# Kernel optimization log

Measured on AMD Instinct MI355X. Metric: run time of the kernel, lower is better.

## Reference

```python
import jax, jax.numpy as jnp
import numpy as np

TOP_K = 2

def setup_inputs() -> dict:
    key = jax.random.key(0)
    k1, k2, k3, k4, k5 = jax.random.split(key, 5)
    B, S, D, E, H = 1, 2048, 2048, 8, 5632
    scale = 0.02
    return {
        "x": jax.random.normal(k1, (B, S, D), dtype=jnp.float32),
        "gate_w": jax.random.normal(k2, (E, D), dtype=jnp.float32) * scale,
        "w1": jax.random.normal(k3, (E, H, D), dtype=jnp.float32) * scale,
        "w2": jax.random.normal(k4, (E, D, H), dtype=jnp.float32) * scale,
        "w3": jax.random.normal(k5, (E, H, D), dtype=jnp.float32) * scale,
    }


def reference(x, gate_w, w1, w2, w3):
    # x: [B, S, D]; gate_w: [E, D]; w1/w3: [E, H, D]; w2: [E, D, H]
    B, S, D = x.shape
    E = gate_w.shape[0]
    xf = x.reshape(-1, D)                      # [T, D]
    T = xf.shape[0]

    # Gate (gate_softmax=False): topk on raw scores, softmax over the top-k
    scores = xf @ gate_w.T                     # [T, E]
    expert_weights, expert_indices = jax.lax.top_k(scores, TOP_K)
    expert_weights = jax.nn.softmax(expert_weights, axis=-1)  # [T, K]

    # Scatter top-k weights to a dense [T, E] combine matrix (zeros elsewhere)
    combine = jnp.zeros((T, E), dtype=xf.dtype).at[
        jnp.arange(T)[:, None], expert_indices
    ].add(expert_weights)

    # SwiGLU FFN per expert, batched over the (small, fixed) expert axis.
    # Math identical to masked dispatch since combine is zero off the top-k.
    h = jax.nn.silu(jnp.einsum("td,ehd->eth", xf, w1)) \
        * jnp.einsum("td,ehd->eth", xf, w3)    # [E, T, H]
    ye = jnp.einsum("eth,edh->etd", h, w2)     # [E, T, D]

    # Weighted combine of top-k expert outputs per token
    y = jnp.einsum("etd,te->td", ye, combine)  # [T, D]
    return y.reshape(B, S, D)
```

## Files before the change

kernel.cpp:

```cpp
#include <hip/hip_runtime.h>
#include <hip/hip_bf16.h>

#define T_TOK 2048
#define DIM   2048
#define NE    8
#define NH    5632

typedef __attribute__((ext_vector_type(4))) float f32x4;
typedef __attribute__((ext_vector_type(8))) short short8;
typedef __attribute__((ext_vector_type(4))) unsigned int u32x4;
typedef __attribute__((ext_vector_type(4))) float float4v;

__device__ inline unsigned short f2bf(float f) {
    unsigned u = __builtin_bit_cast(unsigned, f);
    u += 0x7fffu + ((u >> 16) & 1u);
    return (unsigned short)(u >> 16);
}

__device__ __forceinline__ void glds16(const void* g, void* l) {
    __builtin_amdgcn_global_load_lds((const __attribute__((address_space(1))) void*)g,
                                     (__attribute__((address_space(3))) void*)l, 16, 0, 0);
}

__global__ void k_cvt(const float* __restrict__ src, unsigned short* __restrict__ dst, int n8) {
    int i = blockIdx.x * blockDim.x + threadIdx.x;
    if (i >= n8) return;
    const float4v* xv = (const float4v*)src;
    float4v a = xv[2 * i], b = xv[2 * i + 1];
    short8 o;
    o[0] = (short)f2bf(a[0]); o[1] = (short)f2bf(a[1]);
    o[2] = (short)f2bf(a[2]); o[3] = (short)f2bf(a[3]);
    o[4] = (short)f2bf(b[0]); o[5] = (short)f2bf(b[1]);
    o[6] = (short)f2bf(b[2]); o[7] = (short)f2bf(b[3]);
    ((short8*)dst)[i] = o;
}

__global__ void k_gate(const float* __restrict__ x, const float* __restrict__ gw,
                       int* __restrict__ rt_e, float* __restrict__ rt_w, int* __restrict__ cnt) {
    int wid = threadIdx.x >> 6, lane = threadIdx.x & 63;
    int t = blockIdx.x * 4 + wid;
    if (t >= T_TOK) return;
    float acc[NE];
#pragma unroll
    for (int e = 0; e < NE; e++) acc[e] = 0.f;
    const float* xr = x + (size_t)t * DIM;
    for (int d = lane; d < DIM; d += 64) {
        float xv = xr[d];
#pragma unroll
        for (int e = 0; e < NE; e++) acc[e] += xv * gw[e * DIM + d];
    }
#pragma unroll
    for (int e = 0; e < NE; e++) {
        float v = acc[e];
#pragma unroll
        for (int off = 32; off; off >>= 1) v += __shfl_xor(v, off);
        acc[e] = v;
    }
    if (lane == 0) {
        int i0 = 0; float s0 = acc[0];
#pragma unroll
        for (int e = 1; e < NE; e++) if (acc[e] > s0) { s0 = acc[e]; i0 = e; }
        int i1 = -1; float s1 = -1e30f;
#pragma unroll
        for (int e = 0; e < NE; e++) if (e != i0 && acc[e] > s1) { s1 = acc[e]; i1 = e; }
        float w0 = 1.f / (1.f + expf(s1 - s0));
        rt_e[2 * t] = i0; rt_e[2 * t + 1] = i1;
        rt_w[2 * t] = w0; rt_w[2 * t + 1] = 1.f - w0;
        atomicAdd(&cnt[i0], 1);
        atomicAdd(&cnt[i1], 1);
    }
}

__global__ void k_base(const int* __restrict__ cnt, int* __restrict__ base, int* __restrict__ pb) {
    if (threadIdx.x == 0) {
        int s = 0, p = 0;
        for (int e = 0; e < NE; e++) {
            base[e] = s; pb[e] = p;
            s += cnt[e];
            p += ((cnt[e] + 127) >> 7) << 7;
        }
    }
}

__global__ void k_assign(const int* __restrict__ rt_e, const float* __restrict__ rt_w,
                         const int* __restrict__ base, int* __restrict__ run,
                         int* __restrict__ tok, float* __restrict__ tw) {
    int t = blockIdx.x * blockDim.x + threadIdx.x;
    if (t >= T_TOK) return;
#pragma unroll
    for (int k = 0; k < 2; k++) {
        int e = rt_e[2 * t + k];
        int p = atomicAdd(&run[e], 1);
        int g = base[e] + p;
        tok[g] = t;
        tw[g] = rt_w[2 * t + k];
    }
}

__global__ void k_packw13(const float* __restrict__ w1, const float* __restrict__ w3,
                          unsigned short* __restrict__ w1p, unsigned short* __restrict__ w3p) {
    int z = blockIdx.z;
    const float* src = (z < 8) ? w1 : w3;
    unsigned short* dst = (z < 8) ? w1p : w3p;
    int e = z & 7, nt = blockIdx.y, kt = blockIdx.x;
    int lane = threadIdx.x & 63, w = threadIdx.x >> 6;
    int kc = lane & 7;
    const float* sb = src + (size_t)e * NH * DIM;
    unsigned short* db = dst + ((size_t)(e * 88 + nt) * 32 + kt) * 4096;
#pragma unroll
    for (int it = 0; it < 2; ++it) {
        int rloc = it * 32 + w * 8 + (lane >> 3);
        const float* s = sb + (size_t)(nt * 64 + rloc) * DIM + kt * 64 + kc * 8;
        float4v a = *(const float4v*)s, b = *(const float4v*)(s + 4);
        short8 o;
        o[0]=(short)f2bf(a[0]); o[1]=(short)f2bf(a[1]); o[2]=(short)f2bf(a[2]); o[3]=(short)f2bf(a[3]);
        o[4]=(short)f2bf(b[0]); o[5]=(short)f2bf(b[1]); o[6]=(short)f2bf(b[2]); o[7]=(short)f2bf(b[3]);
        *(short8*)(db + kc * 512 + rloc * 8) = o;
    }
}

__global__ void k_packw2(const float* __restrict__ w2, unsigned short* __restrict__ w2p) {
    int e = blockIdx.z, nt = blockIdx.y, kt = blockIdx.x;
    int lane = threadIdx.x & 63, w = threadIdx.x >> 6;
    int kc = lane & 7;
    const float* sb = w2 + (size_t)e * DIM * NH;
    unsigned short* db = w2p + ((size_t)(e * 16 + nt) * 88 + kt) * 8192;
#pragma unroll
    for (int it = 0; it < 4; ++it) {
        int rloc = it * 32 + w * 8 + (lane >> 3);
        const float* s = sb + (size_t)(nt * 128 + rloc) * NH + kt * 64 + kc * 8;
        float4v a = *(const float4v*)s, b = *(const float4v*)(s + 4);
        short8 o;
        o[0]=(short)f2bf(a[0]); o[1]=(short)f2bf(a[1]); o[2]=(short)f2bf(a[2]); o[3]=(short)f2bf(a[3]);
        o[4]=(short)f2bf(b[0]); o[5]=(short)f2bf(b[1]); o[6]=(short)f2bf(b[2]); o[7]=(short)f2bf(b[3]);
        *(short8*)(db + kc * 1024 + rloc * 8) = o;
    }
}

__global__ void k_xpack(const float* __restrict__ x,
                        const int* __restrict__ cnt, const int* __restrict__ base,
                        const int* __restrict__ pb, const int* __restrict__ tok,
                        unsigned short* __restrict__ xp) {
    int e = blockIdx.z, mt = blockIdx.y, kt = blockIdx.x;
    int c = cnt[e], m0 = mt * 128;
    if (m0 >= c) return;
    int gb = base[e];
    int ptile = (pb[e] >> 7) + mt;
    int lane = threadIdx.x & 63, w = threadIdx.x >> 6;
    int kc = lane & 7;
    unsigned short* db = xp + (size_t)ptile * 262144 + (size_t)kt * 8192;
#pragma unroll
    for (int it = 0; it < 4; ++it) {
        int rloc = it * 32 + w * 8 + (lane >> 3);
        int slot = m0 + rloc;
        int t = tok[gb + (slot < c ? slot : 0)];
        const float* s = x + (size_t)t * DIM + kt * 64 + kc * 8;
        float4v a = *(const float4v*)s, b = *(const float4v*)(s + 4);
        short8 o;
        o[0]=(short)f2bf(a[0]); o[1]=(short)f2bf(a[1]); o[2]=(short)f2bf(a[2]); o[3]=(short)f2bf(a[3]);
        o[4]=(short)f2bf(b[0]); o[5]=(short)f2bf(b[1]); o[6]=(short)f2bf(b[2]); o[7]=(short)f2bf(b[3]);
        *(short8*)(db + kc * 1024 + rloc * 8) = o;
    }
}

__launch_bounds__(256, 4)
__global__ void k_ffn1(const unsigned short* __restrict__ xp,
                       const unsigned short* __restrict__ w1p, const unsigned short* __restrict__ w3p,
                       const int* __restrict__ cnt, const int* __restrict__ pb,
                       unsigned short* __restrict__ hb, int nwg) {
    int bid = blockIdx.x;
    int swz = (bid & 7) * (nwg >> 3) + (bid >> 3);
    int mt = swz & 15;
    int r2 = swz >> 4;
    int nt = r2 % 88;
    int e  = r2 / 88;
    int c  = cnt[e];
    int m0 = mt * 128;
    if (m0 >= c) return;
    int ptile = (pb[e] >> 7) + mt;

    __shared__ unsigned short As[8192];
    __shared__ unsigned short B1[4096];
    __shared__ unsigned short B3[4096];

    int tid = threadIdx.x;
    int lane = tid & 63, w = tid >> 6;
    int wm = w >> 1, wn = w & 1;
    int half = w & 1, wh = w >> 1;

    const unsigned short* aB  = xp  + (size_t)ptile * 262144 + half * 512 + lane * 8;
    const unsigned short* b1B = w1p + (size_t)(e * 88 + nt) * 131072 + lane * 8;
    const unsigned short* b3B = w3p + (size_t)(e * 88 + nt) * 131072 + lane * 8;

    f32x4 acc1[4][2], acc3[4][2];
#pragma unroll
    for (int i = 0; i < 4; i++)
#pragma unroll
        for (int j = 0; j < 2; j++) { acc1[i][j] = (f32x4)0.f; acc3[i][j] = (f32x4)0.f; }

    for (int kt = 0; kt < 32; ++kt) {
        __syncthreads();
#pragma unroll
        for (int i = 0; i < 4; i++) {
            int kc = i * 2 + wh;
            glds16(aB + kt * 8192 + kc * 1024, (char*)As + kc * 2048 + half * 1024);
        }
#pragma unroll
        for (int i = 0; i < 2; i++) {
            int kc = i * 4 + w;
            glds16(b1B + kt * 4096 + kc * 512, (char*)B1 + kc * 1024);
            glds16(b3B + kt * 4096 + kc * 512, (char*)B3 + kc * 1024);
        }
        asm volatile("s_waitcnt vmcnt(0)" ::: "memory");
        __syncthreads();
#pragma unroll
        for (int kh = 0; kh < 2; kh++) {
            int kc = kh * 4 + (lane >> 4);
            short8 a[4], b1[2], b3[2];
#pragma unroll
            for (int mf = 0; mf < 4; mf++) {
                int r = wm * 64 + mf * 16 + (lane & 15);
                a[mf] = *(const short8*)(As + kc * 1024 + r * 8);
            }
#pragma unroll
            for (int nf = 0; nf < 2; nf++) {
                int rb = wn * 32 + nf * 16 + (lane & 15);
                b1[nf] = *(const short8*)(B1 + kc * 512 + rb * 8);
                b3[nf] = *(const short8*)(B3 + kc * 512 + rb * 8);
            }
#pragma unroll
            for (int mf = 0; mf < 4; mf++)
#pragma unroll
                for (int nf = 0; nf < 2; nf++) {
                    acc1[mf][nf] = __builtin_amdgcn_mfma_f32_16x16x32_bf16(a[mf], b1[nf], acc1[mf][nf], 0, 0, 0);
                    acc3[mf][nf] = __builtin_amdgcn_mfma_f32_16x16x32_bf16(a[mf], b3[nf], acc3[mf][nf], 0, 0, 0);
                }
        }
    }

    unsigned short* hT = hb + ((size_t)ptile * 88 + nt) * 8192;
#pragma unroll
    for (int mf = 0; mf < 4; mf++)
#pragma unroll
        for (int nf = 0; nf < 2; nf++)
#pragma unroll
            for (int r = 0; r < 4; r++) {
                int row = wm * 64 + mf * 16 + ((lane >> 4) << 2) + r;
                int col = wn * 32 + nf * 16 + (lane & 15);
                if (m0 + row < c) {
                    float a = acc1[mf][nf][r];
                    float g = a / (1.f + expf(-a));
                    float v = g * acc3[mf][nf][r];
                    hT[(col >> 3) * 1024 + row * 8 + (col & 7)] = f2bf(v);
                }
            }
}

__launch_bounds__(256, 4)
__global__ void k_ffn2(const unsigned short* __restrict__ hb,
                       const unsigned short* __restrict__ w2p,
                       const int* __restrict__ cnt, const int* __restrict__ base,
                       const int* __restrict__ pb,
                       const int* __restrict__ tok, const float* __restrict__ tw,
                       float* __restrict__ y, int nwg) {
    int bid = blockIdx.x;
    int swz = (bid & 7) * (nwg >> 3) + (bid >> 3);
    int mt = swz & 15;
    int r2 = swz >> 4;
    int nt = r2 & 15;
    int e  = r2 >> 4;
    int c  = cnt[e];
    int m0 = mt * 128;
    if (m0 >= c) return;
    int gb = base[e];
    int ptile = (pb[e] >> 7) + mt;
    int n0 = nt * 128;

    __shared__ unsigned short As[8192];
    __shared__ unsigned short Bs[8192];
    __shared__ int   toks[128];
    __shared__ float gws[128];

    int tid = threadIdx.x;
    if (tid < 128) {
        int s = m0 + tid;
        toks[tid] = (s < c) ? tok[gb + s] : 0;
        gws[tid]  = (s < c) ? tw[gb + s] : 0.f;
    }

    int lane = tid & 63, w = tid >> 6;
    int wm = w >> 1, wn = w & 1;
    int half = w & 1, wh = w >> 1;

    const unsigned short* aB = hb  + (size_t)ptile * 720896 + half * 512 + lane * 8;
    const unsigned short* bB = w2p + (size_t)(e * 16 + nt) * 720896 + half * 512 + lane * 8;

    f32x4 acc[4][4];
#pragma unroll
    for (int i = 0; i < 4; i++)
#pragma unroll
        for (int j = 0; j < 4; j++) acc[i][j] = (f32x4)0.f;

    for (int kt = 0; kt < 88; ++kt) {
        __syncthreads();
#pragma unroll
        for (int i = 0; i < 4; i++) {
            int kc = i * 2 + wh;
            glds16(aB + kt * 8192 + kc * 1024, (char*)As + kc * 2048 + half * 1024);
            glds16(bB + kt * 8192 + kc * 1024, (char*)Bs + kc * 2048 + half * 1024);
        }
        asm volatile("s_waitcnt vmcnt(0)" ::: "memory");
        __syncthreads();
#pragma unroll
        for (int kh = 0; kh < 2; kh++) {
            int kc = kh * 4 + (lane >> 4);
            short8 a[4], b[4];
#pragma unroll
            for (int mf = 0; mf < 4; mf++) {
                int r = wm * 64 + mf * 16 + (lane & 15);
                a[mf] = *(const short8*)(As + kc * 1024 + r * 8);
            }
#pragma unroll
            for (int nf = 0; nf < 4; nf++) {
                int rb = wn * 64 + nf * 16 + (lane & 15);
                b[nf] = *(const short8*)(Bs + kc * 1024 + rb * 8);
            }
#pragma unroll
            for (int mf = 0; mf < 4; mf++)
#pragma unroll
                for (int nf = 0; nf < 4; nf++)
                    acc[mf][nf] = __builtin_amdgcn_mfma_f32_16x16x32_bf16(a[mf], b[nf], acc[mf][nf], 0, 0, 0);
        }
    }

#pragma unroll
    for (int mf = 0; mf < 4; mf++)
#pragma unroll
        for (int nf = 0; nf < 4; nf++)
#pragma unroll
            for (int r = 0; r < 4; r++) {
                int row = wm * 64 + mf * 16 + ((lane >> 4) << 2) + r;
                int col = wn * 64 + nf * 16 + (lane & 15);
                if (m0 + row < c) {
                    float v = gws[row] * acc[mf][nf][r];
                    atomicAdd(&y[(size_t)toks[row] * DIM + n0 + col], v);
                }
            }
}

__launch_bounds__(256)
__global__ void k_ffn1_fb(const unsigned short* __restrict__ xb,
                          const float* __restrict__ w1, const float* __restrict__ w3,
                          const int* __restrict__ cnt, const int* __restrict__ base,
                          const int* __restrict__ tok, unsigned short* __restrict__ hbuf) {
    int e  = blockIdx.x >> 4;
    int mt = blockIdx.x & 15;
    int c  = cnt[e];
    int m0 = mt * 128;
    if (m0 >= c) return;
    int gb = base[e];
    int n0 = blockIdx.y * 64;

    __shared__ unsigned short As[128 * 64];
    __shared__ unsigned short B1s[64 * 64];
    __shared__ unsigned short B3s[64 * 64];
    __shared__ int toks[128];

    int tid = threadIdx.x;
    if (tid < 128) {
        int s = m0 + tid;
        toks[tid] = (s < c) ? tok[gb + s] : tok[gb];
    }
    int lane = tid & 63, wid = tid >> 6;
    int wm = wid >> 1, wn = wid & 1;

    f32x4 acc1[4][2], acc3[4][2];
#pragma unroll
    for (int i = 0; i < 4; i++)
#pragma unroll
        for (int j = 0; j < 2; j++) { acc1[i][j] = (f32x4)0.f; acc3[i][j] = (f32x4)0.f; }

    const float* W1 = w1 + (size_t)e * NH * DIM + (size_t)n0 * DIM;
    const float* W3 = w3 + (size_t)e * NH * DIM + (size_t)n0 * DIM;

    for (int kt = 0; kt < DIM / 64; ++kt) {
        int k0 = kt * 64;
        __syncthreads();
#pragma unroll
        for (int i = 0; i < 4; i++) {
            int f = i * 256 + tid;
            int row = f >> 3, ch = f & 7;
            u32x4 v = *(const u32x4*)(xb + (size_t)toks[row] * DIM + k0 + ch * 8);
            *(u32x4*)(As + row * 64 + ((ch ^ (row & 7)) << 3)) = v;
        }
#pragma unroll
        for (int i = 0; i < 2; i++) {
            int f = i * 256 + tid;
            int row = f >> 3, ch = f & 7;
            {
                const float* src = W1 + (size_t)row * DIM + k0 + ch * 8;
                float4v a = *(const float4v*)src, b = *(const float4v*)(src + 4);
                short8 o;
                o[0]=(short)f2bf(a[0]); o[1]=(short)f2bf(a[1]); o[2]=(short)f2bf(a[2]); o[3]=(short)f2bf(a[3]);
                o[4]=(short)f2bf(b[0]); o[5]=(short)f2bf(b[1]); o[6]=(short)f2bf(b[2]); o[7]=(short)f2bf(b[3]);
                *(short8*)(B1s + row * 64 + ((ch ^ (row & 7)) << 3)) = o;
            }
            {
                const float* src = W3 + (size_t)row * DIM + k0 + ch * 8;
                float4v a = *(const float4v*)src, b = *(const float4v*)(src + 4);
                short8 o;
                o[0]=(short)f2bf(a[0]); o[1]=(short)f2bf(a[1]); o[2]=(short)f2bf(a[2]); o[3]=(short)f2bf(a[3]);
                o[4]=(short)f2bf(b[0]); o[5]=(short)f2bf(b[1]); o[6]=(short)f2bf(b[2]); o[7]=(short)f2bf(b[3]);
                *(short8*)(B3s + row * 64 + ((ch ^ (row & 7)) << 3)) = o;
            }
        }
        __syncthreads();
#pragma unroll
        for (int kk = 0; kk < 2; kk++) {
            int kch = kk * 4 + (lane >> 4);
            short8 af[4], b1f[2], b3f[2];
#pragma unroll
            for (int mf = 0; mf < 4; mf++) {
                int r = wm * 64 + mf * 16 + (lane & 15);
                af[mf] = *(const short8*)(As + r * 64 + ((kch ^ (r & 7)) << 3));
            }
#pragma unroll
            for (int nf = 0; nf < 2; nf++) {
                int r = wn * 32 + nf * 16 + (lane & 15);
                b1f[nf] = *(const short8*)(B1s + r * 64 + ((kch ^ (r & 7)) << 3));
                b3f[nf] = *(const short8*)(B3s + r * 64 + ((kch ^ (r & 7)) << 3));
            }
#pragma unroll
            for (int mf = 0; mf < 4; mf++)
#pragma unroll
                for (int nf = 0; nf < 2; nf++) {
                    acc1[mf][nf] = __builtin_amdgcn_mfma_f32_16x16x32_bf16(af[mf], b1f[nf], acc1[mf][nf], 0, 0, 0);
                    acc3[mf][nf] = __builtin_amdgcn_mfma_f32_16x16x32_bf16(af[mf], b3f[nf], acc3[mf][nf], 0, 0, 0);
                }
        }
    }
#pragma unroll
    for (int mf = 0; mf < 4; mf++)
#pragma unroll
        for (int nf = 0; nf < 2; nf++)
#pragma unroll
            for (int r = 0; r < 4; r++) {
                int row = wm * 64 + mf * 16 + ((lane >> 4) << 2) + r;
                int col = wn * 32 + nf * 16 + (lane & 15);
                if (m0 + row < c) {
                    float a = acc1[mf][nf][r];
                    float g = a / (1.f + expf(-a));
                    float v = g * acc3[mf][nf][r];
                    hbuf[(size_t)(gb + m0 + row) * NH + n0 + col] = f2bf(v);
                }
            }
}

__launch_bounds__(256)
__global__ void k_ffn2_fb(const unsigned short* __restrict__ hbuf,
                          const float* __restrict__ w2,
                          const int* __restrict__ cnt, const int* __restrict__ base,
                          const int* __restrict__ tok, const float* __restrict__ tw,
                          float* __restrict__ y) {
    int e  = blockIdx.x >> 4;
    int mt = blockIdx.x & 15;
    int c  = cnt[e];
    int m0 = mt * 128;
    if (m0 >= c) return;
    int gb = base[e];
    int n0 = blockIdx.y * 128;

    __shared__ unsigned short As[128 * 64];
    __shared__ unsigned short Bs[128 * 64];
    __shared__ int   toks[128];
    __shared__ float gws[128];

    int tid = threadIdx.x;
    if (tid < 128) {
        int s = m0 + tid;
        toks[tid] = (s < c) ? tok[gb + s] : 0;
        gws[tid]  = (s < c) ? tw[gb + s] : 0.f;
    }
    int lane = tid & 63, wid = tid >> 6;
    int wm = wid >> 1, wn = wid & 1;

    f32x4 acc[4][4];
#pragma unroll
    for (int i = 0; i < 4; i++)
#pragma unroll
        for (int j = 0; j < 4; j++) acc[i][j] = (f32x4)0.f;

    const float* W2 = w2 + (size_t)e * DIM * NH + (size_t)n0 * NH;

    for (int kt = 0; kt < NH / 64; ++kt) {
        int k0 = kt * 64;
        __syncthreads();
#pragma unroll
        for (int i = 0; i < 4; i++) {
            int f = i * 256 + tid;
            int row = f >> 3, ch = f & 7;
            int rr = m0 + row; rr = (rr < c) ? rr : (c - 1);
            u32x4 v = *(const u32x4*)(hbuf + (size_t)(gb + rr) * NH + k0 + ch * 8);
            *(u32x4*)(As + row * 64 + ((ch ^ (row & 7)) << 3)) = v;
        }
#pragma unroll
        for (int i = 0; i < 4; i++) {
            int f = i * 256 + tid;
            int row = f >> 3, ch = f & 7;
            const float* src = W2 + (size_t)row * NH + k0 + ch * 8;
            float4v a = *(const float4v*)src, b = *(const float4v*)(src + 4);
            short8 o;
            o[0]=(short)f2bf(a[0]); o[1]=(short)f2bf(a[1]); o[2]=(short)f2bf(a[2]); o[3]=(short)f2bf(a[3]);
            o[4]=(short)f2bf(b[0]); o[5]=(short)f2bf(b[1]); o[6]=(short)f2bf(b[2]); o[7]=(short)f2bf(b[3]);
            *(short8*)(Bs + row * 64 + ((ch ^ (row & 7)) << 3)) = o;
        }
        __syncthreads();
#pragma unroll
        for (int kk = 0; kk < 2; kk++) {
            int kch = kk * 4 + (lane >> 4);
            short8 af[4], bf[4];
#pragma unroll
            for (int mf = 0; mf < 4; mf++) {
                int r = wm * 64 + mf * 16 + (lane & 15);
                af[mf] = *(const short8*)(As + r * 64 + ((kch ^ (r & 7)) << 3));
            }
#pragma unroll
            for (int nf = 0; nf < 4; nf++) {
                int r = wn * 64 + nf * 16 + (lane & 15);
                bf[nf] = *(const short8*)(Bs + r * 64 + ((kch ^ (r & 7)) << 3));
            }
#pragma unroll
            for (int mf = 0; mf < 4; mf++)
#pragma unroll
                for (int nf = 0; nf < 4; nf++)
                    acc[mf][nf] = __builtin_amdgcn_mfma_f32_16x16x32_bf16(af[mf], bf[nf], acc[mf][nf], 0, 0, 0);
        }
    }
#pragma unroll
    for (int mf = 0; mf < 4; mf++)
#pragma unroll
        for (int nf = 0; nf < 4; nf++)
#pragma unroll
            for (int r = 0; r < 4; r++) {
                int row = wm * 64 + mf * 16 + ((lane >> 4) << 2) + r;
                int col = wn * 64 + nf * 16 + (lane & 15);
                if (m0 + row < c) {
                    float v = gws[row] * acc[mf][nf][r];
                    atomicAdd(&y[(size_t)toks[row] * DIM + n0 + col], v);
                }
            }
}

extern "C" void kernel_launch(void* const* d_in, const int* in_sizes, int n_in,
                              void* d_out, int out_size, void* d_ws, size_t ws_size,
                              hipStream_t stream) {
    const float* x  = (const float*)d_in[0];
    const float* gw = (const float*)d_in[1];
    const float* w1 = (const float*)d_in[2];
    const float* w2 = (const float*)d_in[3];
    const float* w3 = (const float*)d_in[4];
    float* y = (float*)d_out;

    char* ws = (char*)d_ws;
    int*   cnt  = (int*)(ws + 0);
    int*   run  = (int*)(ws + 64);
    int*   basep= (int*)(ws + 128);
    int*   pb   = (int*)(ws + 192);
    int*   tok  = (int*)(ws + 256);
    float* tw   = (float*)(ws + 16640);
    int*   rt_e = (int*)(ws + 33024);
    float* rt_w = (float*)(ws + 49408);
    unsigned short* xp    = (unsigned short*)(ws + 66048);
    unsigned short* hbufp = (unsigned short*)(ws + 21037568);
    unsigned short* w1p   = (unsigned short*)(ws + 78709248);
    unsigned short* w3p   = (unsigned short*)(ws + 263258624);
    unsigned short* w2p   = (unsigned short*)(ws + 447808000);
    const size_t needed = 632357376ull;

    hipMemsetAsync(ws, 0, 256, stream);
    hipMemsetAsync(d_out, 0, (size_t)out_size * sizeof(float), stream);

    k_gate<<<T_TOK / 4, 256, 0, stream>>>(x, gw, rt_e, rt_w, cnt);
    k_base<<<1, 64, 0, stream>>>(cnt, basep, pb);
    k_assign<<<T_TOK / 256, 256, 0, stream>>>(rt_e, rt_w, basep, run, tok, tw);

    if (ws_size >= needed) {
        k_packw13<<<dim3(32, 88, 16), 256, 0, stream>>>(w1, w3, w1p, w3p);
        k_packw2<<<dim3(88, 16, NE), 256, 0, stream>>>(w2, w2p);
        k_xpack<<<dim3(32, 16, NE), 256, 0, stream>>>(x, cnt, basep, pb, tok, xp);
        int nwg1 = NE * 16 * 88;
        int nwg2 = NE * 16 * 16;
        k_ffn1<<<nwg1, 256, 0, stream>>>(xp, w1p, w3p, cnt, pb, hbufp, nwg1);
        k_ffn2<<<nwg2, 256, 0, stream>>>(hbufp, w2p, cnt, basep, pb, tok, tw, y, nwg2);
    } else {
        k_cvt<<<(T_TOK * DIM / 8) / 256, 256, 0, stream>>>(x, xp, T_TOK * DIM / 8);
        k_ffn1_fb<<<dim3(NE * 16, NH / 64), 256, 0, stream>>>(xp, w1, w3, cnt, basep, tok, hbufp);
        k_ffn2_fb<<<dim3(NE * 16, DIM / 128), 256, 0, stream>>>(hbufp, w2, cnt, basep, tok, tw, y);
    }
}
```

Before: 884.8 us.

## Fuse fp32-to-bf16 weight packing into the FFN GEMM tile loads

Removes the separate weight pre-pack kernels (w1/w3/w2 fp32 to bf16 blocked layout) and instead loads fp32 weights directly in the GEMM inner loop, converting to bf16 in registers before writing to LDS. This avoids writing and re-reading about half a GB of packed weights each call and shrinks the workspace requirement. In exchange, each weight tile is read as fp32 (twice the bytes) by every M-tile workgroup that uses it, and the loads go through registers instead of direct-to-LDS, which may reduce overlap and raise register pressure.

```diff
diff --git a/kernel.cpp b/kernel.cpp
--- a/kernel.cpp
+++ b/kernel.cpp
@@ -17,6 +17,13 @@
     return (unsigned short)(u >> 16);
 }
 
+__device__ __forceinline__ short8 pack8(float4v a, float4v b) {
+    short8 o;
+    o[0]=(short)f2bf(a[0]); o[1]=(short)f2bf(a[1]); o[2]=(short)f2bf(a[2]); o[3]=(short)f2bf(a[3]);
+    o[4]=(short)f2bf(b[0]); o[5]=(short)f2bf(b[1]); o[6]=(short)f2bf(b[2]); o[7]=(short)f2bf(b[3]);
+    return o;
+}
+
 __device__ __forceinline__ void glds16(const void* g, void* l) {
     __builtin_amdgcn_global_load_lds((const __attribute__((address_space(1))) void*)g,
                                      (__attribute__((address_space(3))) void*)l, 16, 0, 0);
@@ -26,13 +33,7 @@
     int i = blockIdx.x * blockDim.x + threadIdx.x;
     if (i >= n8) return;
     const float4v* xv = (const float4v*)src;
-    float4v a = xv[2 * i], b = xv[2 * i + 1];
-    short8 o;
-    o[0] = (short)f2bf(a[0]); o[1] = (short)f2bf(a[1]);
-    o[2] = (short)f2bf(a[2]); o[3] = (short)f2bf(a[3]);
-    o[4] = (short)f2bf(b[0]); o[5] = (short)f2bf(b[1]);
-    o[6] = (short)f2bf(b[2]); o[7] = (short)f2bf(b[3]);
-    ((short8*)dst)[i] = o;
+    ((short8*)dst)[i] = pack8(xv[2 * i], xv[2 * i + 1]);
 }
 
 __global__ void k_gate(const float* __restrict__ x, const float* __restrict__ gw,
@@ -94,46 +95,6 @@
         int g = base[e] + p;
         tok[g] = t;
         tw[g] = rt_w[2 * t + k];
-    }
-}
-
-__global__ void k_packw13(const float* __restrict__ w1, const float* __restrict__ w3,
-                          unsigned short* __restrict__ w1p, unsigned short* __restrict__ w3p) {
-    int z = blockIdx.z;
-    const float* src = (z < 8) ? w1 : w3;
-    unsigned short* dst = (z < 8) ? w1p : w3p;
-    int e = z & 7, nt = blockIdx.y, kt = blockIdx.x;
-    int lane = threadIdx.x & 63, w = threadIdx.x >> 6;
-    int kc = lane & 7;
-    const float* sb = src + (size_t)e * NH * DIM;
-    unsigned short* db = dst + ((size_t)(e * 88 + nt) * 32 + kt) * 4096;
-#pragma unroll
-    for (int it = 0; it < 2; ++it) {
-        int rloc = it * 32 + w * 8 + (lane >> 3);
-        const float* s = sb + (size_t)(nt * 64 + rloc) * DIM + kt * 64 + kc * 8;
-        float4v a = *(const float4v*)s, b = *(const float4v*)(s + 4);
-        short8 o;
-        o[0]=(short)f2bf(a[0]); o[1]=(short)f2bf(a[1]); o[2]=(short)f2bf(a[2]); o[3]=(short)f2bf(a[3]);
-        o[4]=(short)f2bf(b[0]); o[5]=(short)f2bf(b[1]); o[6]=(short)f2bf(b[2]); o[7]=(short)f2bf(b[3]);
-        *(short8*)(db + kc * 512 + rloc * 8) = o;
-    }
-}
-
-__global__ void k_packw2(const float* __restrict__ w2, unsigned short* __restrict__ w2p) {
-    int e = blockIdx.z, nt = blockIdx.y, kt = blockIdx.x;
-    int lane = threadIdx.x & 63, w = threadIdx.x >> 6;
-    int kc = lane & 7;
-    const float* sb = w2 + (size_t)e * DIM * NH;
-    unsigned short* db = w2p + ((size_t)(e * 16 + nt) * 88 + kt) * 8192;
-#pragma unroll
-    for (int it = 0; it < 4; ++it) {
-        int rloc = it * 32 + w * 8 + (lane >> 3);
-        const float* s = sb + (size_t)(nt * 128 + rloc) * NH + kt * 64 + kc * 8;
-        float4v a = *(const float4v*)s, b = *(const float4v*)(s + 4);
-        short8 o;
-        o[0]=(short)f2bf(a[0]); o[1]=(short)f2bf(a[1]); o[2]=(short)f2bf(a[2]); o[3]=(short)f2bf(a[3]);
-        o[4]=(short)f2bf(b[0]); o[5]=(short)f2bf(b[1]); o[6]=(short)f2bf(b[2]); o[7]=(short)f2bf(b[3]);
-        *(short8*)(db + kc * 1024 + rloc * 8) = o;
     }
 }
 
@@ -155,17 +116,13 @@
         int slot = m0 + rloc;
         int t = tok[gb + (slot < c ? slot : 0)];
         const float* s = x + (size_t)t * DIM + kt * 64 + kc * 8;
-        float4v a = *(const float4v*)s, b = *(const float4v*)(s + 4);
-        short8 o;
-        o[0]=(short)f2bf(a[0]); o[1]=(short)f2bf(a[1]); o[2]=(short)f2bf(a[2]); o[3]=(short)f2bf(a[3]);
-        o[4]=(short)f2bf(b[0]); o[5]=(short)f2bf(b[1]); o[6]=(short)f2bf(b[2]); o[7]=(short)f2bf(b[3]);
-        *(short8*)(db + kc * 1024 + rloc * 8) = o;
+        *(short8*)(db + kc * 1024 + rloc * 8) = pack8(*(const float4v*)s, *(const float4v*)(s + 4));
     }
 }
 
 __launch_bounds__(256, 4)
 __global__ void k_ffn1(const unsigned short* __restrict__ xp,
-                       const unsigned short* __restrict__ w1p, const unsigned short* __restrict__ w3p,
+                       const float* __restrict__ w1, const float* __restrict__ w3,
                        const int* __restrict__ cnt, const int* __restrict__ pb,
                        unsigned short* __restrict__ hb, int nwg) {
     int bid = blockIdx.x;
@@ -188,9 +145,13 @@
     int wm = w >> 1, wn = w & 1;
     int half = w & 1, wh = w >> 1;
 
-    const unsigned short* aB  = xp  + (size_t)ptile * 262144 + half * 512 + lane * 8;
-    const unsigned short* b1B = w1p + (size_t)(e * 88 + nt) * 131072 + lane * 8;
-    const unsigned short* b3B = w3p + (size_t)(e * 88 + nt) * 131072 + lane * 8;
+    const unsigned short* aB = xp + (size_t)ptile * 262144 + half * 512 + lane * 8;
+
+    int br  = tid >> 2;
+    int bko = (tid & 3) << 4;
+    int kcb = bko >> 3;
+    const float* w1r = w1 + (size_t)e * NH * DIM + (size_t)(nt * 64 + br) * DIM + bko;
+    const float* w3r = w3 + (size_t)e * NH * DIM + (size_t)(nt * 64 + br) * DIM + bko;
 
     f32x4 acc1[4][2], acc3[4][2];
 #pragma unroll
@@ -205,11 +166,17 @@
             int kc = i * 2 + wh;
             glds16(aB + kt * 8192 + kc * 1024, (char*)As + kc * 2048 + half * 1024);
         }
-#pragma unroll
-        for (int i = 0; i < 2; i++) {
-            int kc = i * 4 + w;
-            glds16(b1B + kt * 4096 + kc * 512, (char*)B1 + kc * 1024);
-            glds16(b3B + kt * 4096 + kc * 512, (char*)B3 + kc * 1024);
+        {
+            const float* s1 = w1r + kt * 64;
+            float4v f0 = *(const float4v*)s1,       f1 = *(const float4v*)(s1 + 4);
+            float4v f2 = *(const float4v*)(s1 + 8), f3 = *(const float4v*)(s1 + 12);
+            *(short8*)(B1 + kcb * 512 + br * 8)       = pack8(f0, f1);
+            *(short8*)(B1 + (kcb + 1) * 512 + br * 8) = pack8(f2, f3);
+            const float* s3 = w3r + kt * 64;
+            float4v g0 = *(const float4v*)s3,       g1 = *(const float4v*)(s3 + 4);
+            float4v g2 = *(const float4v*)(s3 + 8), g3 = *(const float4v*)(s3 + 12);
+            *(short8*)(B3 + kcb * 512 + br * 8)       = pack8(g0, g1);
+            *(short8*)(B3 + (kcb + 1) * 512 + br * 8) = pack8(g2, g3);
         }
         asm volatile("s_waitcnt vmcnt(0)" ::: "memory");
         __syncthreads();
@@ -258,7 +225,7 @@
 
 __launch_bounds__(256, 4)
 __global__ void k_ffn2(const unsigned short* __restrict__ hb,
-                       const unsigned short* __restrict__ w2p,
+                       const float* __restrict__ w2,
                        const int* __restrict__ cnt, const int* __restrict__ base,
                        const int* __restrict__ pb,
                        const int* __restrict__ tok, const float* __restrict__ tw,
@@ -292,8 +259,12 @@
     int wm = w >> 1, wn = w & 1;
     int half = w & 1, wh = w >> 1;
 
-    const unsigned short* aB = hb  + (size_t)ptile * 720896 + half * 512 + lane * 8;
-    const unsigned short* bB = w2p + (size_t)(e * 16 + nt) * 720896 + half * 512 + lane * 8;
+    const unsigned short* aB = hb + (size_t)ptile * 720896 + half * 512 + lane * 8;
+
+    int br  = tid >> 1;
+    int bko = (tid & 1) << 5;
+    int kcb = bko >> 3;
+    const float* w2r = w2 + (size_t)e * DIM * NH + (size_t)(n0 + br) * NH + bko;
 
     f32x4 acc[4][4];
 #pragma unroll
@@ -307,7 +278,17 @@
         for (int i = 0; i < 4; i++) {
             int kc = i * 2 + wh;
             glds16(aB + kt * 8192 + kc * 1024, (char*)As + kc * 2048 + half * 1024);
-            glds16(bB + kt * 8192 + kc * 1024, (char*)Bs + kc * 2048 + half * 1024);
+        }
+        {
+            const float* s = w2r + kt * 64;
+            float4v f0 = *(const float4v*)s,       f1 = *(const float4v*)(s + 4);
+            float4v f2 = *(const float4v*)(s + 8), f3 = *(const float4v*)(s + 12);
+            *(short8*)(Bs + kcb * 1024 + br * 8)       = pack8(f0, f1);
+            *(short8*)(Bs + (kcb + 1) * 1024 + br * 8) = pack8(f2, f3);
+            f0 = *(const float4v*)(s + 16); f1 = *(const float4v*)(s + 20);
+            f2 = *(const float4v*)(s + 24); f3 = *(const float4v*)(s + 28);
+            *(short8*)(Bs + (kcb + 2) * 1024 + br * 8) = pack8(f0, f1);
+            *(short8*)(Bs + (kcb + 3) * 1024 + br * 8) = pack8(f2, f3);
         }
         asm volatile("s_waitcnt vmcnt(0)" ::: "memory");
         __syncthreads();
@@ -399,19 +380,13 @@
             int row = f >> 3, ch = f & 7;
             {
                 const float* src = W1 + (size_t)row * DIM + k0 + ch * 8;
-                float4v a = *(const float4v*)src, b = *(const float4v*)(src + 4);
-                short8 o;
-                o[0]=(short)f2bf(a[0]); o[1]=(short)f2bf(a[1]); o[2]=(short)f2bf(a[2]); o[3]=(short)f2bf(a[3]);
-                o[4]=(short)f2bf(b[0]); o[5]=(short)f2bf(b[1]); o[6]=(short)f2bf(b[2]); o[7]=(short)f2bf(b[3]);
-                *(short8*)(B1s + row * 64 + ((ch ^ (row & 7)) << 3)) = o;
+                *(short8*)(B1s + row * 64 + ((ch ^ (row & 7)) << 3)) =
+                    pack8(*(const float4v*)src, *(const float4v*)(src + 4));
             }
             {
                 const float* src = W3 + (size_t)row * DIM + k0 + ch * 8;
-                float4v a = *(const float4v*)src, b = *(const float4v*)(src + 4);
-                short8 o;
-                o[0]=(short)f2bf(a[0]); o[1]=(short)f2bf(a[1]); o[2]=(short)f2bf(a[2]); o[3]=(short)f2bf(a[3]);
-                o[4]=(short)f2bf(b[0]); o[5]=(short)f2bf(b[1]); o[6]=(short)f2bf(b[2]); o[7]=(short)f2bf(b[3]);
-                *(short8*)(B3s + row * 64 + ((ch ^ (row & 7)) << 3)) = o;
+                *(short8*)(B3s + row * 64 + ((ch ^ (row & 7)) << 3)) =
+                    pack8(*(const float4v*)src, *(const float4v*)(src + 4));
             }
         }
         __syncthreads();
@@ -508,11 +483,8 @@
             int f = i * 256 + tid;
             int row = f >> 3, ch = f & 7;
             const float* src = W2 + (size_t)row * NH + k0 + ch * 8;
-            float4v a = *(const float4v*)src, b = *(const float4v*)(src + 4);
-            short8 o;
-            o[0]=(short)f2bf(a[0]); o[1]=(short)f2bf(a[1]); o[2]=(short)f2bf(a[2]); o[3]=(short)f2bf(a[3]);
-            o[4]=(short)f2bf(b[0]); o[5]=(short)f2bf(b[1]); o[6]=(short)f2bf(b[2]); o[7]=(short)f2bf(b[3]);
-            *(short8*)(Bs + row * 64 + ((ch ^ (row & 7)) << 3)) = o;
+            *(short8*)(Bs + row * 64 + ((ch ^ (row & 7)) << 3)) =
+                pack8(*(const float4v*)src, *(const float4v*)(src + 4));
         }
         __syncthreads();
 #pragma unroll
@@ -572,10 +544,7 @@
     float* rt_w = (float*)(ws + 49408);
     unsigned short* xp    = (unsigned short*)(ws + 66048);
     unsigned short* hbufp = (unsigned short*)(ws + 21037568);
-    unsigned short* w1p   = (unsigned short*)(ws + 78709248);
-    unsigned short* w3p   = (unsigned short*)(ws + 263258624);
-    unsigned short* w2p   = (unsigned short*)(ws + 447808000);
-    const size_t needed = 632357376ull;
+    const size_t needed = 78709248ull;
 
     hipMemsetAsync(ws, 0, 256, stream);
     hipMemsetAsync(d_out, 0, (size_t)out_size * sizeof(float), stream);
@@ -585,13 +554,11 @@
     k_assign<<<T_TOK / 256, 256, 0, stream>>>(rt_e, rt_w, basep, run, tok, tw);
 
     if (ws_size >= needed) {
-        k_packw13<<<dim3(32, 88, 16), 256, 0, stream>>>(w1, w3, w1p, w3p);
-        k_packw2<<<dim3(88, 16, NE), 256, 0, stream>>>(w2, w2p);
         k_xpack<<<dim3(32, 16, NE), 256, 0, stream>>>(x, cnt, basep, pb, tok, xp);
         int nwg1 = NE * 16 * 88;
         int nwg2 = NE * 16 * 16;
-        k_ffn1<<<nwg1, 256, 0, stream>>>(xp, w1p, w3p, cnt, pb, hbufp, nwg1);
-        k_ffn2<<<nwg2, 256, 0, stream>>>(hbufp, w2p, cnt, basep, pb, tok, tw, y, nwg2);
+        k_ffn1<<<nwg1, 256, 0, stream>>>(xp, w1, w3, cnt, pb, hbufp, nwg1);
+        k_ffn2<<<nwg2, 256, 0, stream>>>(hbufp, w2, cnt, basep, pb, tok, tw, y, nwg2);
     } else {
         k_cvt<<<(T_TOK * DIM / 8) / 256, 256, 0, stream>>>(x, xp, T_TOK * DIM / 8);
         k_ffn1_fb<<<dim3(NE * 16, NH / 64), 256, 0, stream>>>(xp, w1, w3, cnt, basep, tok, hbufp);
```

After: 1.206 ms. 36.3% more time.
